# Performance work log

Measured on AMD Instinct MI355X. Metric: run time of the kernel, lower is better.

## Reference

```python
import jax, jax.numpy as jnp
import numpy as np

N, E, IN, ED, OUT = 50000, 800000, 64, 16, 64
AVG_D_LOG = 2.833  # log(avg_degree + 1), avg_degree = 16
EPS = 1e-5         # PNA std epsilon


def setup_inputs() -> dict:
    key = jax.random.key(0)
    ks = jax.random.split(key, 8)
    h = jax.random.normal(ks[0], (N, IN), jnp.float32)
    ef = jax.random.normal(ks[1], (E, ED), jnp.float32)
    snorm_n = jax.random.uniform(ks[2], (N, 1), jnp.float32)
    W_pre = jax.random.normal(ks[3], (2 * IN + ED, IN), jnp.float32) * 0.05
    b_pre = jnp.zeros((IN,), jnp.float32)
    W_post = jax.random.normal(ks[4], (13 * IN, OUT), jnp.float32) * 0.05
    b_post = jnp.zeros((OUT,), jnp.float32)
    src = jax.random.randint(ks[5], (E,), 0, N, dtype=jnp.int32).astype(jnp.int64)
    dst = jax.random.randint(ks[6], (E,), 0, N, dtype=jnp.int32).astype(jnp.int64)
    return dict(h=h, ef=ef, snorm_n=snorm_n, W_pre=W_pre, b_pre=b_pre,
                W_post=W_post, b_post=b_post, src=src, dst=dst)


def reference(h, ef, snorm_n, W_pre, b_pre, W_post, b_post, src, dst):
    # pretrans MLP (1 layer -> single linear, no activation) on per-edge concat
    z = jnp.concatenate([h[src], h[dst], ef], axis=1)      # [E, 2*IN+ED]
    msg = z @ W_pre + b_pre                                # [E, IN]

    deg = jax.ops.segment_sum(jnp.ones((E,), msg.dtype), dst, num_segments=N)  # [N]
    degc = jnp.maximum(deg, 1.0)
    has_msg = (deg > 0)[:, None]

    s = jax.ops.segment_sum(msg, dst, num_segments=N)
    mean = s / degc[:, None]
    mean_sq = jax.ops.segment_sum(msg * msg, dst, num_segments=N) / degc[:, None]
    std = jnp.sqrt(jax.nn.relu(mean_sq - mean * mean) + EPS)
    mx = jax.ops.segment_max(msg, dst, num_segments=N)
    mn = jax.ops.segment_min(msg, dst, num_segments=N)

    agg = jnp.concatenate([mean, mx, mn, std], axis=1)      # [N, 4*IN]
    agg = jnp.where(has_msg, agg, 0.0)                      # zero-in-degree nodes get 0

    logd = jnp.log(degc + 1.0)
    amp = agg * (logd / AVG_D_LOG)[:, None]                 # amplification scaler
    att = agg * (AVG_D_LOG / logd)[:, None]                 # attenuation scaler

    hcat = jnp.concatenate([h, agg, amp, att], axis=1)      # [N, 13*IN]
    out = hcat @ W_post + b_post                            # posttrans MLP (1 layer)
    out = out * snorm_n                                     # graph_norm
    return out
```

## Files before the change

kernel.cpp:

```cpp
#include <hip/hip_runtime.h>

constexpr int N_NODES = 50000;
constexpr int N_EDGES = 800000;
constexpr int IN_F = 64;
constexpr int ED_F = 16;
constexpr int OUT_F = 64;
constexpr int AGG_F = 256;
constexpr int KTOT = 832;
constexpr float AVG_D_LOG_F = 2.833f;
constexpr float EPS_F = 1e-5f;

constexpr int NB_BKT = 256;
constexpr int NODES_PER_BKT = 196;
constexpr int EPB_C = 4096;
constexpr int NBLK_C = (N_EDGES + EPB_C - 1) / EPB_C;

constexpr int AGG_WAVES = 12500;
constexpr int AGG_BLOCKS = AGG_WAVES / 4;

typedef __attribute__((ext_vector_type(8))) short short8;
typedef __attribute__((ext_vector_type(4))) float f32x4;

__device__ __forceinline__ float rl(float v, int l) {
    return __int_as_float(__builtin_amdgcn_readlane(__float_as_int(v), l));
}
__device__ __forceinline__ int rfl(int v) { return __builtin_amdgcn_readfirstlane(v); }
__device__ __forceinline__ unsigned short f2bf(float f) {
    unsigned u = __float_as_uint(f);
    unsigned r = (u + 0x7FFFu + ((u >> 16) & 1u)) >> 16;
    return (unsigned short)r;
}
__device__ __forceinline__ float bf2f(unsigned short s) {
    return __uint_as_float(((unsigned)s) << 16);
}

constexpr int P12MM_BLKS = 625;
constexpr int P12_TPB = 5;
constexpr int HIST_BLKS = (N_EDGES + 255) / 256;
constexpr int HIST_THREADS = HIST_BLKS * 256;
__global__ __launch_bounds__(256) void prep_kernel(
    const float* __restrict__ h, const float* __restrict__ Wpre, const float* __restrict__ bpre,
    const int* __restrict__ dst, const float* __restrict__ ef, const float* __restrict__ Wpost,
    unsigned short* __restrict__ P1b, float* __restrict__ P2, unsigned short* __restrict__ hb,
    int* __restrict__ deg, unsigned short* __restrict__ efb,
    unsigned short* __restrict__ WT, unsigned short* __restrict__ WefT)
{
    int tid = threadIdx.x;
    if (blockIdx.x < P12MM_BLKS) {
        int lane = tid & 63;
        int li = lane & 15;
        int lg = lane >> 4;
        int w = tid >> 6;
        int col = w * 16 + li;

        short8 B1[2], B2[2];
        #pragma unroll
        for (int s = 0; s < 2; ++s) {
            short8 b1 = {}, b2 = {};
            #pragma unroll
            for (int j = 0; j < 8; ++j) {
                int k = s * 32 + (lg << 3) + j;
                b1[j] = (short)f2bf(Wpre[k * 64 + col]);
                b2[j] = (short)f2bf(Wpre[(64 + k) * 64 + col]);
            }
            B1[s] = b1; B2[s] = b2;
        }
        float bj = bpre[col];

        #pragma unroll 1
        for (int t = 0; t < P12_TPB; ++t) {
            int tile = blockIdx.x + t * P12MM_BLKS;
            int nA = tile * 16 + li;
            const float* hrow = h + (size_t)nA * IN_F;
            float4 v0 = *reinterpret_cast<const float4*>(hrow + (lg << 3));
            float4 v1 = *reinterpret_cast<const float4*>(hrow + (lg << 3) + 4);
            float4 v2 = *reinterpret_cast<const float4*>(hrow + 32 + (lg << 3));
            float4 v3 = *reinterpret_cast<const float4*>(hrow + 32 + (lg << 3) + 4);
            short8 a0, a1;
            a0[0]=(short)f2bf(v0.x); a0[1]=(short)f2bf(v0.y); a0[2]=(short)f2bf(v0.z); a0[3]=(short)f2bf(v0.w);
            a0[4]=(short)f2bf(v1.x); a0[5]=(short)f2bf(v1.y); a0[6]=(short)f2bf(v1.z); a0[7]=(short)f2bf(v1.w);
            a1[0]=(short)f2bf(v2.x); a1[1]=(short)f2bf(v2.y); a1[2]=(short)f2bf(v2.z); a1[3]=(short)f2bf(v2.w);
            a1[4]=(short)f2bf(v3.x); a1[5]=(short)f2bf(v3.y); a1[6]=(short)f2bf(v3.z); a1[7]=(short)f2bf(v3.w);

            if (w == 0) {
                *reinterpret_cast<short8*>(hb + (size_t)nA * IN_F + (lg << 3)) = a0;
                *reinterpret_cast<short8*>(hb + (size_t)nA * IN_F + 32 + (lg << 3)) = a1;
            }

            f32x4 p1a = {0.f,0.f,0.f,0.f}, p2a = {0.f,0.f,0.f,0.f};
            p1a = __builtin_amdgcn_mfma_f32_16x16x32_bf16(a0, B1[0], p1a, 0, 0, 0);
            p1a = __builtin_amdgcn_mfma_f32_16x16x32_bf16(a1, B1[1], p1a, 0, 0, 0);
            p2a = __builtin_amdgcn_mfma_f32_16x16x32_bf16(a0, B2[0], p2a, 0, 0, 0);
            p2a = __builtin_amdgcn_mfma_f32_16x16x32_bf16(a1, B2[1], p2a, 0, 0, 0);

            #pragma unroll
            for (int rr = 0; rr < 4; ++rr) {
                int node = tile * 16 + (lg << 2) + rr;
                P1b[(size_t)node * IN_F + col] = f2bf(p1a[rr]);
                P2[(size_t)node * IN_F + col] = p2a[rr] + bj;
            }
        }
    } else {
        int gid = (blockIdx.x - P12MM_BLKS) * 256 + tid;
        if (gid < N_EDGES) atomicAdd(&deg[dst[gid]], 1);
        for (size_t i = gid; i < (size_t)N_EDGES * ED_F; i += HIST_THREADS)
            efb[i] = f2bf(ef[i]);
        if (gid < OUT_F * KTOT) {
            int n = gid / KTOT, k = gid % KTOT;
            WT[gid] = f2bf(Wpost[(size_t)k * OUT_F + n]);
        }
        if (gid < 64 * 16) {
            int n = gid >> 4, k = gid & 15;
            WefT[gid] = f2bf(Wpre[(128 + k) * 64 + n]);
        }
    }
}

constexpr int NBLK_SCAN = (N_NODES + 255) / 256;

__global__ __launch_bounds__(256) void scan1_kernel(const int* __restrict__ deg, int* __restrict__ bsum)
{
    __shared__ int ws[4];
    int tid = threadIdx.x, lane = tid & 63, wv = tid >> 6;
    int i = blockIdx.x * 256 + tid;
    int v = (i < N_NODES) ? deg[i] : 0;
    #pragma unroll
    for (int off = 32; off > 0; off >>= 1) v += __shfl_down(v, off);
    if (lane == 0) ws[wv] = v;
    __syncthreads();
    if (tid == 0) bsum[blockIdx.x] = ws[0] + ws[1] + ws[2] + ws[3];
}

__global__ __launch_bounds__(256) void scan2_kernel(const int* __restrict__ bsum, int* __restrict__ bpre)
{
    __shared__ int ws[4];
    int tid = threadIdx.x, lane = tid & 63, wv = tid >> 6;
    int v = (tid < NBLK_SCAN) ? bsum[tid] : 0;
    int sc = v;
    #pragma unroll
    for (int off = 1; off < 64; off <<= 1) {
        int u = __shfl_up(sc, off);
        if (lane >= off) sc += u;
    }
    if (lane == 63) ws[wv] = sc;
    __syncthreads();
    int wbase = 0;
    #pragma unroll
    for (int w = 0; w < 4; ++w) if (w < wv) wbase += ws[w];
    if (tid < NBLK_SCAN) bpre[tid] = wbase + sc - v;
}

__global__ __launch_bounds__(256) void scan3_kernel(
    const int* __restrict__ deg, const int* __restrict__ bpre,
    int* __restrict__ row_start, int* __restrict__ bcur)
{
    __shared__ int ws[4];
    int tid = threadIdx.x, lane = tid & 63, wv = tid >> 6;
    int i = blockIdx.x * 256 + tid;
    int v = (i < N_NODES) ? deg[i] : 0;
    int sc = v;
    #pragma unroll
    for (int off = 1; off < 64; off <<= 1) {
        int u = __shfl_up(sc, off);
        if (lane >= off) sc += u;
    }
    if (lane == 63) ws[wv] = sc;
    __syncthreads();
    int wbase = 0;
    #pragma unroll
    for (int w = 0; w < 4; ++w) if (w < wv) wbase += ws[w];
    int ex = bpre[blockIdx.x] + wbase + sc - v;
    if (i < N_NODES) {
        row_start[i] = ex;
        int b = i / NODES_PER_BKT;
        if (b * NODES_PER_BKT == i) bcur[b] = ex;
    }
}

__global__ __launch_bounds__(256) void binC_kernel(
    const int* __restrict__ src, const int* __restrict__ dst, int* __restrict__ bcur,
    int* __restrict__ stage_e, int* __restrict__ stage_s, int* __restrict__ stage_d)
{
    __shared__ int sL[EPB_C];
    __shared__ int dL[EPB_C];
    __shared__ int bh[NB_BKT];
    __shared__ int bbase[NB_BKT];
    __shared__ int bcsr[NB_BKT];

    int tid = threadIdx.x;
    int e0 = blockIdx.x * EPB_C;

    bh[tid] = 0;
    __syncthreads();
    #pragma unroll
    for (int k = 0; k < EPB_C / 256; ++k) {
        int t = k * 256 + tid;
        int e = e0 + t;
        if (e < N_EDGES) {
            int s = src[e], d = dst[e];
            sL[t] = s; dL[t] = d;
            atomicAdd(&bh[d / NODES_PER_BKT], 1);
        }
    }
    __syncthreads();
    bbase[tid] = (bh[tid] > 0) ? atomicAdd(&bcur[tid], bh[tid]) : 0;
    bcsr[tid] = 0;
    __syncthreads();
    #pragma unroll
    for (int k = 0; k < EPB_C / 256; ++k) {
        int t = k * 256 + tid;
        int e = e0 + t;
        if (e < N_EDGES) {
            int d = dL[t];
            int b = d / NODES_PER_BKT;
            int r = atomicAdd(&bcsr[b], 1);
            int pos = bbase[b] + r;
            stage_e[pos] = e;
            stage_s[pos] = sL[t];
            stage_d[pos] = d;
        }
    }
}

__global__ __launch_bounds__(256) void binD_kernel(
    const int* __restrict__ stage_e, const int* __restrict__ stage_s,
    const int* __restrict__ stage_d, const int* __restrict__ row_start,
    int2* __restrict__ csr2)
{
    __shared__ int cur[NODES_PER_BKT];
    int tid = threadIdx.x;
    int b = blockIdx.x;
    int nb0 = b * NODES_PER_BKT;
    for (int i = tid; i < NODES_PER_BKT; i += 256) cur[i] = 0;
    __syncthreads();
    int pbeg = row_start[nb0];
    int nb1 = nb0 + NODES_PER_BKT;
    int pend = (nb1 < N_NODES) ? row_start[nb1] : N_EDGES;
    for (int p = pbeg + tid; p < pend; p += 256) {
        int d = stage_d[p];
        int r = atomicAdd(&cur[d - nb0], 1);
        csr2[row_start[d] + r] = make_int2(stage_e[p], stage_s[p]);
    }
}

__global__ __launch_bounds__(256) void aggmm_kernel(
    const unsigned short* __restrict__ P1b, const float* __restrict__ P2,
    const unsigned short* __restrict__ efb, const unsigned short* __restrict__ WefT,
    const int2* __restrict__ csr2, const int* __restrict__ row_start,
    const int* __restrict__ deg, unsigned short* __restrict__ aggb)
{
    int tid = threadIdx.x;
    int lane = tid & 63;
    int lg = lane >> 4;
    int li = lane & 15;

    short8 bI0 = {}, bI1 = {};
    #pragma unroll
    for (int j = 0; j < 8; ++j) {
        int k_local = (lg << 3) + j;
        if (k_local == li)      bI0[j] = (short)0x3F80;
        if (k_local == 16 + li) bI1[j] = (short)0x3F80;
    }
    short8 bE[4];
    #pragma unroll
    for (int ct = 0; ct < 4; ++ct) {
        short8 b = {};
        if (lane < 32)
            b = *reinterpret_cast<const short8*>(WefT + (size_t)(ct * 16 + li) * 16 + (lg << 3));
        bE[ct] = b;
    }

    int wgid = rfl(blockIdx.x * 4 + (tid >> 6));

    #pragma unroll 1
    for (int nn = 0; nn < 4; ++nn) {
        int n = wgid + nn * AGG_WAVES;
        int rs = rfl(row_start[n]);
        int dg = rfl(deg[n]);
        size_t obase = (size_t)n * AGG_F + lane;

        if (dg == 0) {
            aggb[obase] = 0; aggb[obase + 64] = 0;
            aggb[obase + 128] = 0; aggb[obase + 192] = 0;
            continue;
        }

        float p2n = P2[(size_t)n * IN_F + lane];
        const float NINF = -__builtin_inff(), PINF = __builtin_inff();
        float sm[4] = {0.f, 0.f, 0.f, 0.f};
        float sq[4] = {0.f, 0.f, 0.f, 0.f};
        float mx[4] = {NINF, NINF, NINF, NINF};
        float mn[4] = {PINF, PINF, PINF, PINF};

        for (int base = 0; base < dg; base += 64) {
            int cnt = dg - base; if (cnt > 64) cnt = 64;
            int2 es = make_int2(0, 0);
            if (lane < cnt) es = csr2[rs + base + lane];
            int eid = es.x, sid = es.y;
            int nfull = cnt >> 4;

            for (int rt = 0; rt < nfull; ++rt) {
                int srcidx = rt * 16 + li;
                int s_l = __shfl(sid, srcidx);
                int e_l = __shfl(eid, srcidx);
                short8 aP0 = *reinterpret_cast<const short8*>(P1b + (size_t)s_l * IN_F + (lg << 3));
                short8 aP1 = *reinterpret_cast<const short8*>(P1b + (size_t)s_l * IN_F + 32 + (lg << 3));
                short8 aE = {};
                if (lane < 32)
                    aE = *reinterpret_cast<const short8*>(efb + (size_t)e_l * ED_F + (lg << 3));

                f32x4 c0 = {0.f,0.f,0.f,0.f}, c1 = {0.f,0.f,0.f,0.f};
                f32x4 c2 = {0.f,0.f,0.f,0.f}, c3 = {0.f,0.f,0.f,0.f};
                c0 = __builtin_amdgcn_mfma_f32_16x16x32_bf16(aP0, bI0, c0, 0, 0, 0);
                c1 = __builtin_amdgcn_mfma_f32_16x16x32_bf16(aP0, bI1, c1, 0, 0, 0);
                c2 = __builtin_amdgcn_mfma_f32_16x16x32_bf16(aP1, bI0, c2, 0, 0, 0);
                c3 = __builtin_amdgcn_mfma_f32_16x16x32_bf16(aP1, bI1, c3, 0, 0, 0);
                c0 = __builtin_amdgcn_mfma_f32_16x16x32_bf16(aE, bE[0], c0, 0, 0, 0);
                c1 = __builtin_amdgcn_mfma_f32_16x16x32_bf16(aE, bE[1], c1, 0, 0, 0);
                c2 = __builtin_amdgcn_mfma_f32_16x16x32_bf16(aE, bE[2], c2, 0, 0, 0);
                c3 = __builtin_amdgcn_mfma_f32_16x16x32_bf16(aE, bE[3], c3, 0, 0, 0);

                #pragma unroll
                for (int rr = 0; rr < 4; ++rr) {
                    float x0 = c0[rr], x1 = c1[rr], x2 = c2[rr], x3 = c3[rr];
                    sm[0] += x0; sm[1] += x1; sm[2] += x2; sm[3] += x3;
                    sq[0] = fmaf(x0, x0, sq[0]); sq[1] = fmaf(x1, x1, sq[1]);
                    sq[2] = fmaf(x2, x2, sq[2]); sq[3] = fmaf(x3, x3, sq[3]);
                    mx[0] = fmaxf(mx[0], x0); mx[1] = fmaxf(mx[1], x1);
                    mx[2] = fmaxf(mx[2], x2); mx[3] = fmaxf(mx[3], x3);
                    mn[0] = fminf(mn[0], x0); mn[1] = fminf(mn[1], x1);
                    mn[2] = fminf(mn[2], x2); mn[3] = fminf(mn[3], x3);
                }
            }

            if (cnt & 15) {
                int rowb0 = nfull * 16;
                int srcidx = rowb0 + li;
                if (srcidx >= cnt) srcidx = cnt - 1;
                int s_l = __shfl(sid, srcidx);
                int e_l = __shfl(eid, srcidx);
                short8 aP0 = *reinterpret_cast<const short8*>(P1b + (size_t)s_l * IN_F + (lg << 3));
                short8 aP1 = *reinterpret_cast<const short8*>(P1b + (size_t)s_l * IN_F + 32 + (lg << 3));
                short8 aE = {};
                if (lane < 32)
                    aE = *reinterpret_cast<const short8*>(efb + (size_t)e_l * ED_F + (lg << 3));

                f32x4 c0 = {0.f,0.f,0.f,0.f}, c1 = {0.f,0.f,0.f,0.f};
                f32x4 c2 = {0.f,0.f,0.f,0.f}, c3 = {0.f,0.f,0.f,0.f};
                c0 = __builtin_amdgcn_mfma_f32_16x16x32_bf16(aP0, bI0, c0, 0, 0, 0);
                c1 = __builtin_amdgcn_mfma_f32_16x16x32_bf16(aP0, bI1, c1, 0, 0, 0);
                c2 = __builtin_amdgcn_mfma_f32_16x16x32_bf16(aP1, bI0, c2, 0, 0, 0);
                c3 = __builtin_amdgcn_mfma_f32_16x16x32_bf16(aP1, bI1, c3, 0, 0, 0);
                c0 = __builtin_amdgcn_mfma_f32_16x16x32_bf16(aE, bE[0], c0, 0, 0, 0);
                c1 = __builtin_amdgcn_mfma_f32_16x16x32_bf16(aE, bE[1], c1, 0, 0, 0);
                c2 = __builtin_amdgcn_mfma_f32_16x16x32_bf16(aE, bE[2], c2, 0, 0, 0);
                c3 = __builtin_amdgcn_mfma_f32_16x16x32_bf16(aE, bE[3], c3, 0, 0, 0);

                int rb = rowb0 + (lg << 2);
                #pragma unroll
                for (int rr = 0; rr < 4; ++rr) {
                    bool v = (rb + rr) < cnt;
                    float x0 = c0[rr], x1 = c1[rr], x2 = c2[rr], x3 = c3[rr];
                    float z0 = v ? x0 : 0.f, z1 = v ? x1 : 0.f, z2 = v ? x2 : 0.f, z3 = v ? x3 : 0.f;
                    sm[0] += z0; sm[1] += z1; sm[2] += z2; sm[3] += z3;
                    sq[0] = fmaf(z0, z0, sq[0]); sq[1] = fmaf(z1, z1, sq[1]);
                    sq[2] = fmaf(z2, z2, sq[2]); sq[3] = fmaf(z3, z3, sq[3]);
                    mx[0] = fmaxf(mx[0], x0); mx[1] = fmaxf(mx[1], x1);
                    mx[2] = fmaxf(mx[2], x2); mx[3] = fmaxf(mx[3], x3);
                    mn[0] = fminf(mn[0], x0); mn[1] = fminf(mn[1], x1);
                    mn[2] = fminf(mn[2], x2); mn[3] = fminf(mn[3], x3);
                }
            }
        }

        #pragma unroll
        for (int ct = 0; ct < 4; ++ct) {
            #pragma unroll
            for (int off = 16; off <= 32; off <<= 1) {
                sm[ct] += __shfl_xor(sm[ct], off);
                sq[ct] += __shfl_xor(sq[ct], off);
                mx[ct] = fmaxf(mx[ct], __shfl_xor(mx[ct], off));
                mn[ct] = fminf(mn[ct], __shfl_xor(mn[ct], off));
            }
        }
        bool s16 = (lane & 16) != 0, s32 = (lane & 32) != 0;
        float S  = s32 ? (s16 ? sm[3] : sm[2]) : (s16 ? sm[1] : sm[0]);
        float Qq = s32 ? (s16 ? sq[3] : sq[2]) : (s16 ? sq[1] : sq[0]);
        float MX = s32 ? (s16 ? mx[3] : mx[2]) : (s16 ? mx[1] : mx[0]);
        float MN = s32 ? (s16 ? mn[3] : mn[2]) : (s16 ? mn[1] : mn[0]);

        float degc = (float)dg;
        float mean_x = S / degc;
        float sd = sqrtf(fmaxf(Qq / degc - mean_x * mean_x, 0.f) + EPS_F);
        aggb[obase]       = f2bf(mean_x + p2n);
        aggb[obase + 64]  = f2bf(MX + p2n);
        aggb[obase + 128] = f2bf(MN + p2n);
        aggb[obase + 192] = f2bf(sd);
    }
}

constexpr int POST_BLOCKS = 625;
constexpr int TILES_PER_BLOCK = 5;
__global__ __launch_bounds__(256, 2) void postmm_kernel(
    const unsigned short* __restrict__ hb, const float* __restrict__ snorm,
    const unsigned short* __restrict__ WT, const float* __restrict__ bpost,
    const unsigned short* __restrict__ aggb, const int* __restrict__ deg,
    float* __restrict__ out)
{
    int tid = threadIdx.x;
    int lane = tid & 63;
    int li = lane & 15;
    int lg = lane >> 4;
    int w = tid >> 6;

    const unsigned short* Brow = WT + (size_t)(w * 16 + li) * KTOT + (lg << 3);
    short8 B[26];
    #pragma unroll
    for (int s = 0; s < 26; ++s)
        B[s] = *reinterpret_cast<const short8*>(Brow + s * 32);

    float bp = bpost[w * 16 + li];

    #pragma unroll 1
    for (int t = 0; t < TILES_PER_BLOCK; ++t) {
        int tile = blockIdx.x + t * POST_BLOCKS;
        int nA = tile * 16 + li;
        const unsigned short* Ah = hb + (size_t)nA * IN_F + (lg << 3);
        const unsigned short* Ag = aggb + (size_t)nA * AGG_F + (lg << 3);

        short8 ah0 = *reinterpret_cast<const short8*>(Ah);
        short8 ah1 = *reinterpret_cast<const short8*>(Ah + 32);
        short8 ag[8];
        #pragma unroll
        for (int s = 0; s < 8; ++s)
            ag[s] = *reinterpret_cast<const short8*>(Ag + s * 32);

        f32x4 accA = {0.f,0.f,0.f,0.f}, accB = {0.f,0.f,0.f,0.f}, accC = {0.f,0.f,0.f,0.f};
        accA = __builtin_amdgcn_mfma_f32_16x16x32_bf16(ah0, B[0], accA, 0, 0, 0);
        accA = __builtin_amdgcn_mfma_f32_16x16x32_bf16(ah1, B[1], accA, 0, 0, 0);
        #pragma unroll
        for (int s = 0; s < 8; ++s) {
            accA = __builtin_amdgcn_mfma_f32_16x16x32_bf16(ag[s], B[2 + s],  accA, 0, 0, 0);
            accB = __builtin_amdgcn_mfma_f32_16x16x32_bf16(ag[s], B[10 + s], accB, 0, 0, 0);
            accC = __builtin_amdgcn_mfma_f32_16x16x32_bf16(ag[s], B[18 + s], accC, 0, 0, 0);
        }

        #pragma unroll
        for (int rr = 0; rr < 4; ++rr) {
            int node = tile * 16 + (lg << 2) + rr;
            int dg = deg[node];
            float degc = fmaxf((float)dg, 1.f);
            float logd = logf(degc + 1.f);
            float aR = logd * (1.f / AVG_D_LOG_F);
            float bR = AVG_D_LOG_F / logd;
            float v = accA[rr] + aR * accB[rr] + bR * accC[rr] + bp;
            out[(size_t)node * OUT_F + w * 16 + li] = v * snorm[node];
        }
    }
}

extern "C" void kernel_launch(void* const* d_in, const int* in_sizes, int n_in,
                              void* d_out, int out_size, void* d_ws, size_t ws_size,
                              hipStream_t stream) {
    const float* h     = (const float*)d_in[0];
    const float* ef    = (const float*)d_in[1];
    const float* snorm = (const float*)d_in[2];
    const float* Wpre  = (const float*)d_in[3];
    const float* bpre  = (const float*)d_in[4];
    const float* Wpost = (const float*)d_in[5];
    const float* bpost = (const float*)d_in[6];
    const int* src     = (const int*)d_in[7];
    const int* dst     = (const int*)d_in[8];
    float* out = (float*)d_out;

    char* ws = (char*)d_ws;
    size_t off = 0;
    auto alloc = [&](size_t bytes) { char* p = ws + off; off += (bytes + 255) & ~size_t(255); return p; };
    unsigned short* P1b  = (unsigned short*)alloc((size_t)N_NODES * IN_F * 2);
    float* P2            = (float*)alloc((size_t)N_NODES * IN_F * 4);
    unsigned short* hb   = (unsigned short*)alloc((size_t)N_NODES * IN_F * 2);
    unsigned short* aggb = (unsigned short*)alloc((size_t)N_NODES * AGG_F * 2);
    unsigned short* efb  = (unsigned short*)alloc((size_t)N_EDGES * ED_F * 2);
    int* deg       = (int*)alloc((size_t)N_NODES * 4);
    int* row_start = (int*)alloc((size_t)N_NODES * 4);
    int2* csr2     = (int2*)alloc((size_t)N_EDGES * 8);
    int* stage_e   = (int*)alloc((size_t)N_EDGES * 4);
    int* stage_s   = (int*)alloc((size_t)N_EDGES * 4);
    int* stage_d   = (int*)alloc((size_t)N_EDGES * 4);
    int* bcur      = (int*)alloc((size_t)NB_BKT * 4);
    int* bsum      = (int*)alloc((size_t)NBLK_SCAN * 4);
    int* bpre2     = (int*)alloc((size_t)NBLK_SCAN * 4);
    unsigned short* WT   = (unsigned short*)alloc((size_t)OUT_F * KTOT * 2);
    unsigned short* WefT = (unsigned short*)alloc((size_t)64 * 16 * 2);

    hipMemsetAsync(deg, 0, (size_t)N_NODES * 4, stream);
    hipLaunchKernelGGL(prep_kernel, dim3(P12MM_BLKS + HIST_BLKS), dim3(256), 0, stream,
                       h, Wpre, bpre, dst, ef, Wpost,
                       P1b, P2, hb, deg, efb, WT, WefT);
    hipLaunchKernelGGL(scan1_kernel, dim3(NBLK_SCAN), dim3(256), 0, stream, deg, bsum);
    hipLaunchKernelGGL(scan2_kernel, dim3(1), dim3(256), 0, stream, bsum, bpre2);
    hipLaunchKernelGGL(scan3_kernel, dim3(NBLK_SCAN), dim3(256), 0, stream, deg, bpre2, row_start, bcur);
    hipLaunchKernelGGL(binC_kernel, dim3(NBLK_C), dim3(256), 0, stream,
                       src, dst, bcur, stage_e, stage_s, stage_d);
    hipLaunchKernelGGL(binD_kernel, dim3(NB_BKT), dim3(256), 0, stream,
                       stage_e, stage_s, stage_d, row_start, csr2);
    hipLaunchKernelGGL(aggmm_kernel, dim3(AGG_BLOCKS), dim3(256), 0, stream,
                       P1b, P2, efb, WefT, csr2, row_start, deg, aggb);
    hipLaunchKernelGGL(postmm_kernel, dim3(POST_BLOCKS), dim3(256), 0, stream,
                       hb, snorm, WT, bpost, aggb, deg, out);
}
```

Baseline: 158.9 us.

## Replace per-node degree histogram and 3-kernel scan with bucket histogram and in-bucket scan

Per-node degree counting with global atomics and the three-kernel global scan are replaced by a per-bucket histogram built in shared memory, a single-block scan over 256 buckets, and per-node degree and row_start computed inside binD through a local shared-memory count and scan. The ef-to-bf16 conversion also moves to dedicated blocks that use float4 vector loads. This removes two kernel launches and 800k global atomics, at the cost of binD reading stage_d twice.

```diff
diff --git a/kernel.cpp b/kernel.cpp
--- a/kernel.cpp
+++ b/kernel.cpp
@@ -21,28 +21,22 @@
 typedef __attribute__((ext_vector_type(8))) short short8;
 typedef __attribute__((ext_vector_type(4))) float f32x4;
 
-__device__ __forceinline__ float rl(float v, int l) {
-    return __int_as_float(__builtin_amdgcn_readlane(__float_as_int(v), l));
-}
 __device__ __forceinline__ int rfl(int v) { return __builtin_amdgcn_readfirstlane(v); }
 __device__ __forceinline__ unsigned short f2bf(float f) {
     unsigned u = __float_as_uint(f);
     unsigned r = (u + 0x7FFFu + ((u >> 16) & 1u)) >> 16;
     return (unsigned short)r;
 }
-__device__ __forceinline__ float bf2f(unsigned short s) {
-    return __uint_as_float(((unsigned)s) << 16);
-}
 
 constexpr int P12MM_BLKS = 625;
 constexpr int P12_TPB = 5;
-constexpr int HIST_BLKS = (N_EDGES + 255) / 256;
-constexpr int HIST_THREADS = HIST_BLKS * 256;
+constexpr int BKT_BLKS = 196;
+constexpr int CONV_BLKS = 2500;
 __global__ __launch_bounds__(256) void prep_kernel(
     const float* __restrict__ h, const float* __restrict__ Wpre, const float* __restrict__ bpre,
     const int* __restrict__ dst, const float* __restrict__ ef, const float* __restrict__ Wpost,
     unsigned short* __restrict__ P1b, float* __restrict__ P2, unsigned short* __restrict__ hb,
-    int* __restrict__ deg, unsigned short* __restrict__ efb,
+    int* __restrict__ bktcnt, unsigned short* __restrict__ efb,
     unsigned short* __restrict__ WT, unsigned short* __restrict__ WefT)
 {
     int tid = threadIdx.x;
@@ -100,42 +94,46 @@
                 P2[(size_t)node * IN_F + col] = p2a[rr] + bj;
             }
         }
+    } else if (blockIdx.x < P12MM_BLKS + BKT_BLKS) {
+        __shared__ int bh[NB_BKT];
+        bh[tid] = 0;
+        __syncthreads();
+        int e0 = (blockIdx.x - P12MM_BLKS) * EPB_C;
+        #pragma unroll
+        for (int k = 0; k < EPB_C / 256; ++k) {
+            int e = e0 + k * 256 + tid;
+            if (e < N_EDGES) atomicAdd(&bh[dst[e] / NODES_PER_BKT], 1);
+        }
+        __syncthreads();
+        if (bh[tid] > 0) atomicAdd(&bktcnt[tid], bh[tid]);
     } else {
-        int gid = (blockIdx.x - P12MM_BLKS) * 256 + tid;
-        if (gid < N_EDGES) atomicAdd(&deg[dst[gid]], 1);
-        for (size_t i = gid; i < (size_t)N_EDGES * ED_F; i += HIST_THREADS)
-            efb[i] = f2bf(ef[i]);
-        if (gid < OUT_F * KTOT) {
-            int n = gid / KTOT, k = gid % KTOT;
-            WT[gid] = f2bf(Wpost[(size_t)k * OUT_F + n]);
-        }
-        if (gid < 64 * 16) {
-            int n = gid >> 4, k = gid & 15;
-            WefT[gid] = f2bf(Wpre[(128 + k) * 64 + n]);
-        }
-    }
-}
-
-constexpr int NBLK_SCAN = (N_NODES + 255) / 256;
-
-__global__ __launch_bounds__(256) void scan1_kernel(const int* __restrict__ deg, int* __restrict__ bsum)
+        int cgid = (blockIdx.x - P12MM_BLKS - BKT_BLKS) * 256 + tid;
+        const float4* ef4 = reinterpret_cast<const float4*>(ef);
+        #pragma unroll
+        for (int k = 0; k < 5; ++k) {
+            int i = cgid + k * (CONV_BLKS * 256);
+            float4 v = ef4[i];
+            ushort4 o;
+            o.x = f2bf(v.x); o.y = f2bf(v.y); o.z = f2bf(v.z); o.w = f2bf(v.w);
+            *reinterpret_cast<ushort4*>(efb + (size_t)i * 4) = o;
+        }
+        if (cgid < OUT_F * KTOT) {
+            int n = cgid / KTOT, k = cgid % KTOT;
+            WT[cgid] = f2bf(Wpost[(size_t)k * OUT_F + n]);
+        }
+        if (cgid < 64 * 16) {
+            int n = cgid >> 4, k = cgid & 15;
+            WefT[cgid] = f2bf(Wpre[(128 + k) * 64 + n]);
+        }
+    }
+}
+
+__global__ __launch_bounds__(256) void bscan_kernel(
+    const int* __restrict__ bktcnt, int* __restrict__ bkt_start, int* __restrict__ bcur)
 {
     __shared__ int ws[4];
     int tid = threadIdx.x, lane = tid & 63, wv = tid >> 6;
-    int i = blockIdx.x * 256 + tid;
-    int v = (i < N_NODES) ? deg[i] : 0;
-    #pragma unroll
-    for (int off = 32; off > 0; off >>= 1) v += __shfl_down(v, off);
-    if (lane == 0) ws[wv] = v;
-    __syncthreads();
-    if (tid == 0) bsum[blockIdx.x] = ws[0] + ws[1] + ws[2] + ws[3];
-}
-
-__global__ __launch_bounds__(256) void scan2_kernel(const int* __restrict__ bsum, int* __restrict__ bpre)
-{
-    __shared__ int ws[4];
-    int tid = threadIdx.x, lane = tid & 63, wv = tid >> 6;
-    int v = (tid < NBLK_SCAN) ? bsum[tid] : 0;
+    int v = bktcnt[tid];
     int sc = v;
     #pragma unroll
     for (int off = 1; off < 64; off <<= 1) {
@@ -147,34 +145,10 @@
     int wbase = 0;
     #pragma unroll
     for (int w = 0; w < 4; ++w) if (w < wv) wbase += ws[w];
-    if (tid < NBLK_SCAN) bpre[tid] = wbase + sc - v;
-}
-
-__global__ __launch_bounds__(256) void scan3_kernel(
-    const int* __restrict__ deg, const int* __restrict__ bpre,
-    int* __restrict__ row_start, int* __restrict__ bcur)
-{
-    __shared__ int ws[4];
-    int tid = threadIdx.x, lane = tid & 63, wv = tid >> 6;
-    int i = blockIdx.x * 256 + tid;
-    int v = (i < N_NODES) ? deg[i] : 0;
-    int sc = v;
-    #pragma unroll
-    for (int off = 1; off < 64; off <<= 1) {
-        int u = __shfl_up(sc, off);
-        if (lane >= off) sc += u;
-    }
-    if (lane == 63) ws[wv] = sc;
-    __syncthreads();
-    int wbase = 0;
-    #pragma unroll
-    for (int w = 0; w < 4; ++w) if (w < wv) wbase += ws[w];
-    int ex = bpre[blockIdx.x] + wbase + sc - v;
-    if (i < N_NODES) {
-        row_start[i] = ex;
-        int b = i / NODES_PER_BKT;
-        if (b * NODES_PER_BKT == i) bcur[b] = ex;
-    }
+    int ex = wbase + sc - v;
+    bkt_start[tid] = ex;
+    bcur[tid] = ex;
+    if (tid == 255) bkt_start[256] = ex + v;
 }
 
 __global__ __launch_bounds__(256) void binC_kernel(
@@ -224,22 +198,45 @@
 
 __global__ __launch_bounds__(256) void binD_kernel(
     const int* __restrict__ stage_e, const int* __restrict__ stage_s,
-    const int* __restrict__ stage_d, const int* __restrict__ row_start,
-    int2* __restrict__ csr2)
+    const int* __restrict__ stage_d, const int* __restrict__ bkt_start,
+    int* __restrict__ deg, int* __restrict__ row_start, int2* __restrict__ csr2)
 {
-    __shared__ int cur[NODES_PER_BKT];
-    int tid = threadIdx.x;
+    __shared__ int cnt[NB_BKT];
+    __shared__ int lofs[NODES_PER_BKT];
+    __shared__ int ws[4];
+    int tid = threadIdx.x, lane = tid & 63, wv = tid >> 6;
     int b = blockIdx.x;
     int nb0 = b * NODES_PER_BKT;
-    for (int i = tid; i < NODES_PER_BKT; i += 256) cur[i] = 0;
-    __syncthreads();
-    int pbeg = row_start[nb0];
-    int nb1 = nb0 + NODES_PER_BKT;
-    int pend = (nb1 < N_NODES) ? row_start[nb1] : N_EDGES;
+    cnt[tid] = 0;
+    __syncthreads();
+    int pbeg = bkt_start[b];
+    int pend = bkt_start[b + 1];
+    for (int p = pbeg + tid; p < pend; p += 256)
+        atomicAdd(&cnt[stage_d[p] - nb0], 1);
+    __syncthreads();
+    int v = cnt[tid];
+    int sc = v;
+    #pragma unroll
+    for (int off = 1; off < 64; off <<= 1) {
+        int u = __shfl_up(sc, off);
+        if (lane >= off) sc += u;
+    }
+    if (lane == 63) ws[wv] = sc;
+    __syncthreads();
+    int wbase = 0;
+    #pragma unroll
+    for (int w = 0; w < 4; ++w) if (w < wv) wbase += ws[w];
+    int ex = wbase + sc - v;
+    if (tid < NODES_PER_BKT) {
+        int n = nb0 + tid;
+        if (n < N_NODES) { deg[n] = v; row_start[n] = pbeg + ex; }
+        lofs[tid] = pbeg + ex;
+    }
+    __syncthreads();
     for (int p = pbeg + tid; p < pend; p += 256) {
         int d = stage_d[p];
-        int r = atomicAdd(&cur[d - nb0], 1);
-        csr2[row_start[d] + r] = make_int2(stage_e[p], stage_s[p]);
+        int r = atomicAdd(&lofs[d - nb0], 1);
+        csr2[r] = make_int2(stage_e[p], stage_s[p]);
     }
 }
 
@@ -359,9 +356,9 @@
                 int rb = rowb0 + (lg << 2);
                 #pragma unroll
                 for (int rr = 0; rr < 4; ++rr) {
-                    bool v = (rb + rr) < cnt;
+                    bool vv = (rb + rr) < cnt;
                     float x0 = c0[rr], x1 = c1[rr], x2 = c2[rr], x3 = c3[rr];
-                    float z0 = v ? x0 : 0.f, z1 = v ? x1 : 0.f, z2 = v ? x2 : 0.f, z3 = v ? x3 : 0.f;
+                    float z0 = vv ? x0 : 0.f, z1 = vv ? x1 : 0.f, z2 = vv ? x2 : 0.f, z3 = vv ? x3 : 0.f;
                     sm[0] += z0; sm[1] += z1; sm[2] += z2; sm[3] += z3;
                     sq[0] = fmaf(z0, z0, sq[0]); sq[1] = fmaf(z1, z1, sq[1]);
                     sq[2] = fmaf(z2, z2, sq[2]); sq[3] = fmaf(z3, z3, sq[3]);
@@ -487,23 +484,21 @@
     int* stage_e   = (int*)alloc((size_t)N_EDGES * 4);
     int* stage_s   = (int*)alloc((size_t)N_EDGES * 4);
     int* stage_d   = (int*)alloc((size_t)N_EDGES * 4);
+    int* bktcnt    = (int*)alloc((size_t)NB_BKT * 4);
+    int* bkt_start = (int*)alloc((size_t)(NB_BKT + 1) * 4);
     int* bcur      = (int*)alloc((size_t)NB_BKT * 4);
-    int* bsum      = (int*)alloc((size_t)NBLK_SCAN * 4);
-    int* bpre2     = (int*)alloc((size_t)NBLK_SCAN * 4);
     unsigned short* WT   = (unsigned short*)alloc((size_t)OUT_F * KTOT * 2);
     unsigned short* WefT = (unsigned short*)alloc((size_t)64 * 16 * 2);
 
-    hipMemsetAsync(deg, 0, (size_t)N_NODES * 4, stream);
-    hipLaunchKernelGGL(prep_kernel, dim3(P12MM_BLKS + HIST_BLKS), dim3(256), 0, stream,
+    hipMemsetAsync(bktcnt, 0, (size_t)NB_BKT * 4, stream);
+    hipLaunchKernelGGL(prep_kernel, dim3(P12MM_BLKS + BKT_BLKS + CONV_BLKS), dim3(256), 0, stream,
                        h, Wpre, bpre, dst, ef, Wpost,
-                       P1b, P2, hb, deg, efb, WT, WefT);
-    hipLaunchKernelGGL(scan1_kernel, dim3(NBLK_SCAN), dim3(256), 0, stream, deg, bsum);
-    hipLaunchKernelGGL(scan2_kernel, dim3(1), dim3(256), 0, stream, bsum, bpre2);
-    hipLaunchKernelGGL(scan3_kernel, dim3(NBLK_SCAN), dim3(256), 0, stream, deg, bpre2, row_start, bcur);
+                       P1b, P2, hb, bktcnt, efb, WT, WefT);
+    hipLaunchKernelGGL(bscan_kernel, dim3(1), dim3(256), 0, stream, bktcnt, bkt_start, bcur);
     hipLaunchKernelGGL(binC_kernel, dim3(NBLK_C), dim3(256), 0, stream,
                        src, dst, bcur, stage_e, stage_s, stage_d);
     hipLaunchKernelGGL(binD_kernel, dim3(NB_BKT), dim3(256), 0, stream,
-                       stage_e, stage_s, stage_d, row_start, csr2);
+                       stage_e, stage_s, stage_d, bkt_start, deg, row_start, csr2);
     hipLaunchKernelGGL(aggmm_kernel, dim3(AGG_BLOCKS), dim3(256), 0, stream,
                        P1b, P2, efb, WefT, csr2, row_start, deg, aggb);
     hipLaunchKernelGGL(postmm_kernel, dim3(POST_BLOCKS), dim3(256), 0, stream,
```

Result: faster. 137.0 us (-13.8%).
